# Kernel tuning notes

Measured on AMD Instinct MI355X. Metric: run time of the kernel, lower is better.

The kernel has to match this reference:

```python
import jax, jax.numpy as jnp
import numpy as np


def setup_inputs() -> dict:
    key = jax.random.key(0)
    k1, k2, k3, k4 = jax.random.split(key, 4)
    N, F_in, F_out = 8192, 512, 256
    inp = jax.random.normal(k1, (N, F_in), dtype=jnp.float32)
    adj = jax.random.uniform(k2, (N, N), dtype=jnp.float32)
    stdv = 1.0 / np.sqrt(F_out)
    weight = jax.random.uniform(k3, (F_in, F_out), minval=-stdv, maxval=stdv, dtype=jnp.float32)
    b = jax.random.uniform(k4, (F_out,), minval=-stdv, maxval=stdv, dtype=jnp.float32)
    return {"input": inp, "adj": adj, "weight": weight, "b": b}


def reference(input, adj, weight, b):
    N = adj.shape[0]
    degree = jnp.sum(adj, axis=1)                      # [N]
    # A_tilde = 2*I - adj
    A_tilde = 2.0 * jnp.eye(N, dtype=adj.dtype) - adj
    d_inv_sqrt = 1.0 / jnp.sqrt(2.0 + degree)          # [N]
    # D^-1/2 @ A_tilde @ D^-1/2 as broadcasted row/col scaling (same math, O(N^2))
    L_sharpen = d_inv_sqrt[:, None] * A_tilde * d_inv_sqrt[None, :]
    support = input @ weight                           # [N, F_out]
    out = L_sharpen @ support + b                      # [N, F_out]
    return jax.nn.relu(out)
```

## Files before the change

kernel.cpp:

```cpp
#include <hip/hip_runtime.h>


typedef _Float16 h4 __attribute__((ext_vector_type(4)));
typedef _Float16 h8 __attribute__((ext_vector_type(8)));
typedef float f4 __attribute__((ext_vector_type(4)));

__device__ __forceinline__ void gload_lds16(const void* g, void* l) {
    __builtin_amdgcn_global_load_lds(
        (const __attribute__((address_space(1))) void*)g,
        (__attribute__((address_space(3))) void*)l, 16, 0, 0);
}

__device__ __forceinline__ void gload2(const float* p, f4& x, f4& y) {
    asm volatile("global_load_dwordx4 %0, %2, off\n\t"
                 "global_load_dwordx4 %1, %2, off offset:16"
                 : "=&v"(x), "=&v"(y)
                 : "v"(p)
                 : "memory");
}

__global__ __launch_bounds__(256) void k0_wt(const float* __restrict__ weight,
                                             char* __restrict__ wt) {
    const int idx = blockIdx.x * 256 + threadIdx.x;
    const int k = idx >> 8, j = idx & 255;
    const _Float16 h = (_Float16)weight[idx];
    const int off = j * 1024 + ((k >> 6) << 7) + (((k & 63) << 1) ^ ((j & 7) << 4));
    *(_Float16*)(wt + off) = h;
}

__global__ __launch_bounds__(256) void k1_deg(const float* __restrict__ adj,
                                              float* __restrict__ dinv) {
    const int r = blockIdx.x;
    const float4* rp = (const float4*)(adj + (size_t)r * 8192);
    const int t = threadIdx.x;
    float s = 0.f;
#pragma unroll
    for (int i = 0; i < 8; ++i) {
        float4 v = rp[t + i * 256];
        s += (v.x + v.y) + (v.z + v.w);
    }
#pragma unroll
    for (int off = 32; off > 0; off >>= 1) s += __shfl_down(s, off, 64);
    __shared__ float part[4];
    if ((t & 63) == 0) part[t >> 6] = s;
    __syncthreads();
    if (t == 0) {
        float deg = (part[0] + part[1]) + (part[2] + part[3]);
        dinv[r] = 1.0f / sqrtf(2.0f + deg);
    }
}

__global__ __launch_bounds__(512) void k2_support(const float* __restrict__ input,
                                                  const char* __restrict__ wt,
                                                  const float* __restrict__ dinv,
                                                  char* __restrict__ sT) {
    __shared__ char smem[4096 + 32768];
    const int t = threadIdx.x, w = t >> 6, l = t & 63;
    const int r0 = (int)blockIdx.x * 32;
    const int arow = t >> 4, ak4 = t & 15;
    const int bj = l >> 3, bb = (l & 7) * 16;

    f4 acc[2][2] = {};

    for (int kt = 0; kt < 8; ++kt) {
        const int k0 = kt * 64;
        __syncthreads();
        {
            float4 v = *(const float4*)(input + (size_t)(r0 + arow) * 512 + k0 + ak4 * 4);
            h4 h;
            h[0] = (_Float16)v.x; h[1] = (_Float16)v.y;
            h[2] = (_Float16)v.z; h[3] = (_Float16)v.w;
            *(h4*)(smem + arow * 128 + ((ak4 * 8) ^ ((arow & 7) << 4)));
            *(h4*)(smem + arow * 128 + ((ak4 * 8) ^ ((arow & 7) << 4))) = h;
        }
#pragma unroll
        for (int q = 0; q < 4; ++q) {
            const int c = q * 8 + w;
            gload_lds16(wt + (size_t)(c * 8 + bj) * 1024 + kt * 128 + bb,
                        smem + 4096 + c * 1024);
        }
        __syncthreads();
#pragma unroll
        for (int kk = 0; kk < 2; ++kk) {
            const int ko = kk * 64 + ((l >> 4) << 4);
            h8 a[2], b[2];
#pragma unroll
            for (int m = 0; m < 2; ++m) {
                const int r = m * 16 + (l & 15);
                a[m] = *(const h8*)(smem + r * 128 + (ko ^ ((r & 7) << 4)));
            }
#pragma unroll
            for (int n = 0; n < 2; ++n) {
                const int j = w * 32 + n * 16 + (l & 15);
                b[n] = *(const h8*)(smem + 4096 + j * 128 + (ko ^ ((j & 7) << 4)));
            }
#pragma unroll
            for (int m = 0; m < 2; ++m)
#pragma unroll
                for (int n = 0; n < 2; ++n)
                    acc[m][n] = __builtin_amdgcn_mfma_f32_16x16x32_f16(a[m], b[n], acc[m][n], 0, 0, 0);
        }
    }
#pragma unroll
    for (int m = 0; m < 2; ++m)
#pragma unroll
        for (int n = 0; n < 2; ++n) {
            const int j = w * 32 + n * 16 + (l & 15);
            const int k0r = r0 + m * 16 + ((l >> 4) << 2);
            h4 h;
#pragma unroll
            for (int r = 0; r < 2; ++r) h[r] = (_Float16)(dinv[k0r + r] * acc[m][n][r]);
#pragma unroll
            for (int r = 2; r < 4; ++r) h[r] = (_Float16)(dinv[k0r + r] * acc[m][n][r]);
            const int off = j * 16384 + ((k0r >> 6) << 7) +
                            (((k0r & 63) << 1) ^ ((j & 7) << 4));
            *(h4*)(sT + off) = h;
        }
}

__global__ __launch_bounds__(512, 4) void k3_spmm(const float* __restrict__ adj,
                                                  const char* __restrict__ sT,
                                                  float* __restrict__ part,
                                                  float* __restrict__ out,
                                                  int steps) {
    __shared__ __align__(16) char smem[2][40960];
    const int t = threadIdx.x;
    const int w = t >> 6, l = t & 63;
    const int wm = w >> 2, wn = w & 3;
    const int i0 = (int)blockIdx.x * 64;
    const int ks0 = (int)blockIdx.y * steps * 64;
    const int dkt = (i0 - ks0) >> 6;

    const int arow = t >> 3;
    const int ak8 = (t & 7) * 8;
    const int arow_g = i0 + arow;
    const float* aptr = adj + (size_t)arow_g * 8192 + ks0 + ak8;
    const int a_off = arow * 128 + (((t & 7) << 4) ^ ((arow & 7) << 4));

    const int bj = l >> 3, bb = (l & 7) * 16;
    const int chunk0 = ks0 >> 6;

    f4 acc[2][4] = {};

    auto stageB = [&](int kt, char* buf) {
        char* bl = buf + 8192;
#pragma unroll
        for (int q = 0; q < 4; ++q) {
            const int c = w * 4 + q;
            gload_lds16(sT + (size_t)(c * 8 + bj) * 16384 + (chunk0 + kt) * 128 + bb,
                        bl + c * 1024);
        }
    };
    auto writeA = [&](char* buf, int kt, const f4 x, const f4 y) {
        const int kg = ks0 + kt * 64 + ak8;
        h8 h;
        if (kt == dkt) {
#pragma unroll
            for (int e = 0; e < 4; ++e)
                h[e] = (_Float16)((arow_g == kg + e) ? 2.0f - x[e] : -x[e]);
#pragma unroll
            for (int e = 0; e < 4; ++e)
                h[4 + e] = (_Float16)((arow_g == kg + 4 + e) ? 2.0f - y[e] : -y[e]);
        } else {
#pragma unroll
            for (int e = 0; e < 4; ++e) h[e] = (_Float16)(-x[e]);
#pragma unroll
            for (int e = 0; e < 4; ++e) h[4 + e] = (_Float16)(-y[e]);
        }
        *(h8*)(buf + a_off) = h;
    };
    auto compute = [&](const char* buf) {
        const char* A = buf;
        const char* B = buf + 8192;
#pragma unroll
        for (int kk = 0; kk < 2; ++kk) {
            const int ko = kk * 64 + ((l >> 4) << 4);
            h8 a[2], b[4];
#pragma unroll
            for (int m = 0; m < 2; ++m) {
                const int r = wm * 32 + m * 16 + (l & 15);
                a[m] = *(const h8*)(A + r * 128 + (ko ^ ((r & 7) << 4)));
            }
#pragma unroll
            for (int n = 0; n < 4; ++n) {
                const int j = wn * 64 + n * 16 + (l & 15);
                b[n] = *(const h8*)(B + j * 128 + (ko ^ ((j & 7) << 4)));
            }
#pragma unroll
            for (int m = 0; m < 2; ++m)
#pragma unroll
                for (int n = 0; n < 4; ++n)
                    acc[m][n] = __builtin_amdgcn_mfma_f32_16x16x32_f16(a[m], b[n], acc[m][n], 0, 0, 0);
        }
    };

    f4 fx0, fy0, fx1, fy1;

    gload2(aptr, fx0, fy0);
    gload2(aptr + 64, fx1, fy1);
    stageB(0, smem[0]);
    asm volatile("s_waitcnt vmcnt(6)" : "+v"(fx0), "+v"(fy0) :: "memory");
    __builtin_amdgcn_sched_barrier(0);
    writeA(smem[0], 0, fx0, fy0);
    asm volatile("s_waitcnt vmcnt(2) lgkmcnt(0)\n\ts_barrier" ::: "memory");
    __builtin_amdgcn_sched_barrier(0);

    auto body = [&](int kt, f4& xc, f4& yc, f4& xn, f4& yn, char* bufC, char* bufN) {
        stageB(kt + 1, bufN);
        gload2(aptr + (size_t)(kt + 2) * 64, xc, yc);
        asm volatile("s_waitcnt vmcnt(6)" : "+v"(xn), "+v"(yn) :: "memory");
        __builtin_amdgcn_sched_barrier(0);
        writeA(bufN, kt + 1, xn, yn);
        compute(bufC);
        asm volatile("s_waitcnt vmcnt(2) lgkmcnt(0)\n\ts_barrier" ::: "memory");
        __builtin_amdgcn_sched_barrier(0);
    };

    for (int kt2 = 0; kt2 + 2 < steps; kt2 += 2) {
        body(kt2,     fx0, fy0, fx1, fy1, smem[0], smem[1]);
        body(kt2 + 1, fx1, fy1, fx0, fy0, smem[1], smem[0]);
    }
    {
        stageB(steps - 1, smem[1]);
        asm volatile("s_waitcnt vmcnt(4)" : "+v"(fx1), "+v"(fy1) :: "memory");
        __builtin_amdgcn_sched_barrier(0);
        writeA(smem[1], steps - 1, fx1, fy1);
        compute(smem[0]);
        asm volatile("s_waitcnt vmcnt(0) lgkmcnt(0)\n\ts_barrier" ::: "memory");
        __builtin_amdgcn_sched_barrier(0);
        compute(smem[1]);
    }

    float* dst = (blockIdx.y == gridDim.y - 1) ? out
               : part + (size_t)blockIdx.y * (8192 * 256);
#pragma unroll
    for (int m = 0; m < 2; ++m)
#pragma unroll
        for (int n = 0; n < 4; ++n) {
            const int j = wn * 64 + n * 16 + (l & 15);
            const int ib = i0 + wm * 32 + m * 16 + ((l >> 4) << 2);
#pragma unroll
            for (int r = 0; r < 4; ++r)
                dst[(size_t)(ib + r) * 256 + j] = acc[m][n][r];
        }
}

__global__ __launch_bounds__(256) void k4_fin(const float* __restrict__ part,
                                              float* __restrict__ out,
                                              const float* __restrict__ dinv,
                                              const float* __restrict__ bias,
                                              int nsplit) {
    const int idx = blockIdx.x * 256 + threadIdx.x;
    float4 s = ((const float4*)out)[idx];
    for (int sp = 0; sp < nsplit - 1; ++sp)
        s += ((const float4*)(part + (size_t)sp * (8192 * 256)))[idx];
    const float dv = dinv[idx >> 6];
    const float4 b = ((const float4*)bias)[idx & 63];
    float4 r;
    r.x = fmaxf(dv * s.x + b.x, 0.f);
    r.y = fmaxf(dv * s.y + b.y, 0.f);
    r.z = fmaxf(dv * s.z + b.z, 0.f);
    r.w = fmaxf(dv * s.w + b.w, 0.f);
    ((float4*)out)[idx] = r;
}

extern "C" void kernel_launch(void* const* d_in, const int* in_sizes, int n_in,
                              void* d_out, int out_size, void* d_ws, size_t ws_size,
                              hipStream_t stream) {
    const float* input  = (const float*)d_in[0];
    const float* adj    = (const float*)d_in[1];
    const float* weight = (const float*)d_in[2];
    const float* bias   = (const float*)d_in[3];
    float* out = (float*)d_out;

    char* ws = (char*)d_ws;
    float* dinv = (float*)ws;
    char*  wt   = ws + 32768;
    char*  sT   = ws + 294912;
    float* part = (float*)(ws + 294912 + 4194304);

    const size_t base = 294912 + 4194304;
    int nsplit = 1;
    if (ws_size >= base + 3 * 8388608) nsplit = 4;
    else if (ws_size >= base + 1 * 8388608) nsplit = 2;
    const int steps = 128 / nsplit;

    k0_wt<<<512, 256, 0, stream>>>(weight, wt);
    k1_deg<<<8192, 256, 0, stream>>>(adj, dinv);
    k2_support<<<256, 512, 0, stream>>>(input, wt, dinv, sT);
    k3_spmm<<<dim3(128, nsplit), 512, 0, stream>>>(adj, sT, part, out, steps);
    k4_fin<<<2048, 256, 0, stream>>>(part, out, dinv, bias, nsplit);
}
```

Baseline: 137.7 us.

## Load spmm B fragments directly into registers instead of staging through LDS

The spmm kernel now reads the transposed support matrix fragments straight from global memory into registers, using an unswizzled row-major layout written by the support kernel. Only the adjacency tile is staged in LDS, which shrinks shared memory per block from 80KB to 16KB and raises possible occupancy. The warp tiling changes so each wave owns 32 output columns across all 64 rows, so A fragments are shared via LDS and B stays private to each wave. The risk is more global/L2 traffic for B and exposed load latency, since B is loaded in the same iteration it is consumed.

```diff
diff --git a/kernel.cpp b/kernel.cpp
--- a/kernel.cpp
+++ b/kernel.cpp
@@ -14,6 +14,13 @@
 __device__ __forceinline__ void gload2(const float* p, f4& x, f4& y) {
     asm volatile("global_load_dwordx4 %0, %2, off\n\t"
                  "global_load_dwordx4 %1, %2, off offset:16"
+                 : "=&v"(x), "=&v"(y)
+                 : "v"(p)
+                 : "memory");
+}
+__device__ __forceinline__ void gloadB2(const char* p, h8& x, h8& y) {
+    asm volatile("global_load_dwordx4 %0, %2, off\n\t"
+                 "global_load_dwordx4 %1, %2, off offset:64"
                  : "=&v"(x), "=&v"(y)
                  : "v"(p)
                  : "memory");
@@ -70,7 +77,6 @@
             h4 h;
             h[0] = (_Float16)v.x; h[1] = (_Float16)v.y;
             h[2] = (_Float16)v.z; h[3] = (_Float16)v.w;
-            *(h4*)(smem + arow * 128 + ((ak4 * 8) ^ ((arow & 7) << 4)));
             *(h4*)(smem + arow * 128 + ((ak4 * 8) ^ ((arow & 7) << 4))) = h;
         }
 #pragma unroll
@@ -109,12 +115,9 @@
             const int k0r = r0 + m * 16 + ((l >> 4) << 2);
             h4 h;
 #pragma unroll
-            for (int r = 0; r < 2; ++r) h[r] = (_Float16)(dinv[k0r + r] * acc[m][n][r]);
-#pragma unroll
-            for (int r = 2; r < 4; ++r) h[r] = (_Float16)(dinv[k0r + r] * acc[m][n][r]);
-            const int off = j * 16384 + ((k0r >> 6) << 7) +
-                            (((k0r & 63) << 1) ^ ((j & 7) << 4));
-            *(h4*)(sT + off) = h;
+            for (int r = 0; r < 4; ++r)
+                h[r] = (_Float16)(dinv[k0r + r] * acc[m][n][r]);
+            *(h4*)(sT + (size_t)j * 16384 + (size_t)k0r * 2) = h;
         }
 }
 
@@ -123,10 +126,9 @@
                                                   float* __restrict__ part,
                                                   float* __restrict__ out,
                                                   int steps) {
-    __shared__ __align__(16) char smem[2][40960];
+    __shared__ __align__(16) char smem[2][8192];
     const int t = threadIdx.x;
     const int w = t >> 6, l = t & 63;
-    const int wm = w >> 2, wn = w & 3;
     const int i0 = (int)blockIdx.x * 64;
     const int ks0 = (int)blockIdx.y * steps * 64;
     const int dkt = (i0 - ks0) >> 6;
@@ -137,19 +139,18 @@
     const float* aptr = adj + (size_t)arow_g * 8192 + ks0 + ak8;
     const int a_off = arow * 128 + (((t & 7) << 4) ^ ((arow & 7) << 4));
 
-    const int bj = l >> 3, bb = (l & 7) * 16;
-    const int chunk0 = ks0 >> 6;
-
-    f4 acc[2][4] = {};
-
-    auto stageB = [&](int kt, char* buf) {
-        char* bl = buf + 8192;
-#pragma unroll
-        for (int q = 0; q < 4; ++q) {
-            const int c = w * 4 + q;
-            gload_lds16(sT + (size_t)(c * 8 + bj) * 16384 + (chunk0 + kt) * 128 + bb,
-                        bl + c * 1024);
-        }
+    const char* bp0 = sT + ((size_t)(w * 32 + (l & 15)) * 8192 + ks0 + ((l >> 4) << 3)) * 2;
+    const char* bp1 = bp0 + (size_t)16 * 16384;
+
+    f4 acc[4][2] = {};
+    h8 bv[2][2];
+    f4 ax0, ay0, ax1, ay1;
+
+    auto loadB = [&](int kt) {
+        gloadB2(bp0 + (size_t)kt * 128, bv[0][0], bv[1][0]);
+        gloadB2(bp1 + (size_t)kt * 128, bv[0][1], bv[1][1]);
+    };
+    auto waitB = [&]() {
     };
     auto writeA = [&](char* buf, int kt, const f4 x, const f4 y) {
         const int kg = ks0 + kt * 64 + ak8;
@@ -169,76 +170,83 @@
         }
         *(h8*)(buf + a_off) = h;
     };
-    auto compute = [&](const char* buf) {
-        const char* A = buf;
-        const char* B = buf + 8192;
+    auto compute = [&](const char* A) {
 #pragma unroll
         for (int kk = 0; kk < 2; ++kk) {
             const int ko = kk * 64 + ((l >> 4) << 4);
-            h8 a[2], b[4];
-#pragma unroll
-            for (int m = 0; m < 2; ++m) {
-                const int r = wm * 32 + m * 16 + (l & 15);
+            h8 a[4];
+#pragma unroll
+            for (int m = 0; m < 4; ++m) {
+                const int r = m * 16 + (l & 15);
                 a[m] = *(const h8*)(A + r * 128 + (ko ^ ((r & 7) << 4)));
             }
 #pragma unroll
-            for (int n = 0; n < 4; ++n) {
-                const int j = wn * 64 + n * 16 + (l & 15);
-                b[n] = *(const h8*)(B + j * 128 + (ko ^ ((j & 7) << 4)));
-            }
-#pragma unroll
-            for (int m = 0; m < 2; ++m)
-#pragma unroll
-                for (int n = 0; n < 4; ++n)
-                    acc[m][n] = __builtin_amdgcn_mfma_f32_16x16x32_f16(a[m], b[n], acc[m][n], 0, 0, 0);
+            for (int m = 0; m < 4; ++m)
+#pragma unroll
+                for (int n = 0; n < 2; ++n)
+                    acc[m][n] = __builtin_amdgcn_mfma_f32_16x16x32_f16(a[m], bv[kk][n], acc[m][n], 0, 0, 0);
         }
     };
 
-    f4 fx0, fy0, fx1, fy1;
-
-    gload2(aptr, fx0, fy0);
-    gload2(aptr + 64, fx1, fy1);
-    stageB(0, smem[0]);
-    asm volatile("s_waitcnt vmcnt(6)" : "+v"(fx0), "+v"(fy0) :: "memory");
+#define WAIT_ADJ(N, X, Y)                                                     \
+    asm volatile("s_waitcnt vmcnt(" #N ")" : "+v"(X), "+v"(Y) :: "memory");   \
     __builtin_amdgcn_sched_barrier(0);
-    writeA(smem[0], 0, fx0, fy0);
-    asm volatile("s_waitcnt vmcnt(2) lgkmcnt(0)\n\ts_barrier" ::: "memory");
+#define WAIT_B(N)                                                             \
+    asm volatile("s_waitcnt vmcnt(" #N ")"                                    \
+                 : "+v"(bv[0][0]), "+v"(bv[0][1]), "+v"(bv[1][0]), "+v"(bv[1][1]) \
+                 :: "memory");                                                \
     __builtin_amdgcn_sched_barrier(0);
-
-    auto body = [&](int kt, f4& xc, f4& yc, f4& xn, f4& yn, char* bufC, char* bufN) {
-        stageB(kt + 1, bufN);
-        gload2(aptr + (size_t)(kt + 2) * 64, xc, yc);
-        asm volatile("s_waitcnt vmcnt(6)" : "+v"(xn), "+v"(yn) :: "memory");
-        __builtin_amdgcn_sched_barrier(0);
-        writeA(bufN, kt + 1, xn, yn);
-        compute(bufC);
-        asm volatile("s_waitcnt vmcnt(2) lgkmcnt(0)\n\ts_barrier" ::: "memory");
-        __builtin_amdgcn_sched_barrier(0);
-    };
-
-    for (int kt2 = 0; kt2 + 2 < steps; kt2 += 2) {
-        body(kt2,     fx0, fy0, fx1, fy1, smem[0], smem[1]);
-        body(kt2 + 1, fx1, fy1, fx0, fy0, smem[1], smem[0]);
+#define BARRIER()                                                             \
+    asm volatile("s_waitcnt lgkmcnt(0)\n\ts_barrier" ::: "memory");           \
+    __builtin_amdgcn_sched_barrier(0);
+
+    gload2(aptr, ax0, ay0);
+    gload2(aptr + 64, ax1, ay1);
+    WAIT_ADJ(2, ax0, ay0)
+    writeA(smem[0], 0, ax0, ay0);
+    BARRIER()
+
+#define BODY(kt, XC, YC, XN, YN, BUFC, BUFN)                                  \
+    {                                                                         \
+        loadB(kt);                                                            \
+        gload2(aptr + (size_t)(kt + 2) * 64, XC, YC);                         \
+        WAIT_ADJ(6, XN, YN)                                                   \
+        writeA(BUFN, (kt) + 1, XN, YN);                                       \
+        WAIT_B(2)                                                             \
+        compute(BUFC);                                                        \
+        BARRIER()                                                             \
+    }
+
+    for (int kt2 = 0; kt2 + 3 <= steps; kt2 += 2) {
+        BODY(kt2,     ax0, ay0, ax1, ay1, smem[0], smem[1])
+        BODY(kt2 + 1, ax1, ay1, ax0, ay0, smem[1], smem[0])
     }
     {
-        stageB(steps - 1, smem[1]);
-        asm volatile("s_waitcnt vmcnt(4)" : "+v"(fx1), "+v"(fy1) :: "memory");
-        __builtin_amdgcn_sched_barrier(0);
-        writeA(smem[1], steps - 1, fx1, fy1);
+        loadB(steps - 2);
+        WAIT_ADJ(4, ax1, ay1)
+        writeA(smem[1], steps - 1, ax1, ay1);
+        WAIT_B(0)
         compute(smem[0]);
-        asm volatile("s_waitcnt vmcnt(0) lgkmcnt(0)\n\ts_barrier" ::: "memory");
-        __builtin_amdgcn_sched_barrier(0);
+        BARRIER()
+    }
+    {
+        loadB(steps - 1);
+        WAIT_B(0)
         compute(smem[1]);
     }
+#undef BODY
+#undef WAIT_ADJ
+#undef WAIT_B
+#undef BARRIER
 
     float* dst = (blockIdx.y == gridDim.y - 1) ? out
                : part + (size_t)blockIdx.y * (8192 * 256);
 #pragma unroll
-    for (int m = 0; m < 2; ++m)
-#pragma unroll
-        for (int n = 0; n < 4; ++n) {
-            const int j = wn * 64 + n * 16 + (l & 15);
-            const int ib = i0 + wm * 32 + m * 16 + ((l >> 4) << 2);
+    for (int m = 0; m < 4; ++m)
+#pragma unroll
+        for (int n = 0; n < 2; ++n) {
+            const int j = w * 32 + n * 16 + (l & 15);
+            const int ib = i0 + m * 16 + ((l >> 4) << 2);
 #pragma unroll
             for (int r = 0; r < 4; ++r)
                 dst[(size_t)(ib + r) * 256 + j] = acc[m][n][r];
```

After: 149.6 us. 1.09x slower.
